# Performance work log

Measured on AMD Instinct MI355X. Metric: run time of the kernel, lower is better.

The kernel has to match this reference:

```python
import jax, jax.numpy as jnp
import numpy as np

B, L, N, H, D, TOPK = 32, 720, 512, 16, 64, 8
TEMP = 1.0


def setup_inputs() -> dict:
    key = jax.random.key(0)
    ks = jax.random.split(key, 18)
    s = lambda k, shp, fan: jax.random.normal(k, shp, jnp.float32) / np.sqrt(fan)
    return {
        'x': jax.random.normal(ks[0], (B, L, N), jnp.float32),
        'var_embed': s(ks[1], (N, H), H),
        'Wq': s(ks[2], (H, H), H), 'bq': jnp.zeros((H,), jnp.float32),
        'Wk': s(ks[3], (H, H), H), 'bk': jnp.zeros((H,), jnp.float32),
        'Wscore': s(ks[4], (N, 1), N), 'bscore': jnp.zeros((1,), jnp.float32),
        'Wc1': s(ks[5], (N, D), N), 'bc1': jnp.zeros((D,), jnp.float32),
        'Wc2': s(ks[6], (D, D), D), 'bc2': jnp.zeros((D,), jnp.float32),
        'Wcn': s(ks[7], (D, N), D), 'bcn': jnp.zeros((N,), jnp.float32),
        'Wg': s(ks[8], (2 * N, N), 2 * N), 'bg': jnp.zeros((N,), jnp.float32),
        'Wf': s(ks[9], (N, N), N), 'bf': jnp.zeros((N,), jnp.float32),
        'gamma': jnp.ones((N,), jnp.float32), 'beta': jnp.zeros((N,), jnp.float32),
    }


def _forward(x, var_embed, Wq, bq, Wk, bk, Wscore, bscore, Wc1, bc1, Wc2, bc2,
             Wcn, bcn, Wg, bg, Wf, bf, gamma, beta):
    # --- SparseVariableRouter (eval mode: no gumbel noise) ---
    Q = var_embed @ Wq + bq          # [N,H]
    K = var_embed @ Wk + bk          # [N,H]
    sim = Q @ K.T                    # [N,N] (identical across batch in torch)
    eye = jnp.eye(N, dtype=bool)
    sim = jnp.where(eye, -1e9, sim)
    topk_vals, topk_idx = jax.lax.top_k(sim, TOPK)      # [N,k]
    w = jax.nn.softmax(topk_vals / TEMP, axis=-1)        # [N,k]
    x_perm = jnp.transpose(x, (0, 2, 1))                 # [B,N,L]
    neighbors = x_perm[:, topk_idx, :]                   # [B,N,k,L] gather
    ring_out = jnp.einsum('bnkl,nk->bln', neighbors, w)  # [B,L,N]
    # --- center path ---
    attn = jax.nn.softmax(x @ Wscore + bscore, axis=1)   # [B,L,1] softmax over L
    center_raw = jnp.sum(x * attn, axis=1)               # [B,N]
    c = jax.nn.gelu(center_raw @ Wc1 + bc1, approximate=False)
    c = jax.nn.gelu(c @ Wc2 + bc2, approximate=False)
    center = c @ Wcn + bcn                               # [B,N]
    center_b = jnp.broadcast_to(center[:, None, :], (x.shape[0], x.shape[1], N))
    # --- gated fusion + residual LN ---
    gate = jax.nn.sigmoid(jnp.concatenate([ring_out, center_b], axis=-1) @ Wg + bg)
    fused = gate * ring_out + (1.0 - gate) * center_b
    fused = fused @ Wf + bf
    h = fused + x
    mu = jnp.mean(h, axis=-1, keepdims=True)
    var = jnp.var(h, axis=-1, keepdims=True)
    return (h - mu) * jax.lax.rsqrt(var + 1e-5) * gamma + beta


def reference(x, var_embed, Wq, bq, Wk, bk, Wscore, bscore, Wc1, bc1, Wc2, bc2,
              Wcn, bcn, Wg, bg, Wf, bf, gamma, beta):
    return _forward(x, var_embed, Wq, bq, Wk, bk, Wscore, bscore, Wc1, bc1,
                    Wc2, bc2, Wcn, bcn, Wg, bg, Wf, bf, gamma, beta)
```

## Files before the change

### kernel.cpp

```cpp
#include <hip/hip_runtime.h>
#include <hip/hip_bf16.h>
#include <math.h>

#define B_ 32
#define L_ 720
#define N_ 512
#define H_ 16
#define D_ 64
#define TOPK_ 8
#define M_ (B_ * L_)
#define RPB 8
#define CRCH 16
#define CRL (L_ / CRCH)
#define OROWS 32

typedef __bf16 bf16x8 __attribute__((ext_vector_type(8)));
typedef float f32x16 __attribute__((ext_vector_type(16)));

__device__ __forceinline__ void async_cp16(const __hip_bfloat16* g, __hip_bfloat16* l) {
    __builtin_amdgcn_global_load_lds(
        (const __attribute__((address_space(1))) void*)g,
        (__attribute__((address_space(3))) void*)l, 16, 0, 0);
}

__device__ __forceinline__ bf16x8 frag_ld(const __hip_bfloat16* base, int row, int j0) {
    return *(const bf16x8*)(base + row * 64 + (((j0) ^ (row & 7)) << 3));
}

__device__ __forceinline__ f32x16 fzero16() {
    f32x16 z;
    #pragma unroll
    for (int e = 0; e < 16; ++e) z[e] = 0.f;
    return z;
}

__global__ __launch_bounds__(512) void prep_kernel(
    const float* __restrict__ Wg, const float* __restrict__ Wf,
    __hip_bfloat16* __restrict__ WgT, __hip_bfloat16* __restrict__ WfPk,
    const float* __restrict__ ve,
    const float* __restrict__ Wq, const float* __restrict__ bq,
    const float* __restrict__ Wk, const float* __restrict__ bk,
    float* __restrict__ Qm, float* __restrict__ Km)
{
    const int bx = blockIdx.x;
    if (bx < 512) {
        const int n = bx;
        const int k = threadIdx.x;
        WgT[n * N_ + k] = __float2bfloat16(Wg[(size_t)k * N_ + n]);
        const int cblk = n >> 5;
        const int ks32 = k >> 4;
        const int l    = (n & 31) + 32 * ((k >> 3) & 1);
        WfPk[(((size_t)cblk * 32 + ks32) * 64 + l) * 8 + (k & 7)] =
            __float2bfloat16(Wf[(size_t)k * N_ + n]);
    } else {
        const int g = (bx - 512) * 512 + threadIdx.x;
        const int j = g >> 4, h = g & 15;
        const float* vr = ve + j * H_;
        float q = bq[h], k = bk[h];
        #pragma unroll
        for (int m = 0; m < H_; ++m) {
            const float v = vr[m];
            q += v * Wq[m * H_ + h];
            k += v * Wk[m * H_ + h];
        }
        Qm[g] = q;
        Km[g] = k;
    }
}

__global__ __launch_bounds__(64) void topk_kernel(
    const float* __restrict__ Qm, const float* __restrict__ Km,
    float* __restrict__ w_out, int* __restrict__ idx_out)
{
    const int n = blockIdx.x;
    const int lane = threadIdx.x;

    float4 q0, q1, q2, q3;
    {
        const float4* qr = (const float4*)(Qm + n * H_);
        q0 = qr[0]; q1 = qr[1]; q2 = qr[2]; q3 = qr[3];
    }

    float sv[8]; int si[8];
    #pragma unroll
    for (int c = 0; c < 8; ++c) {
        const int j = c * 64 + lane;
        const float4* kr = (const float4*)(Km + j * H_);
        float4 k0 = kr[0], k1 = kr[1], k2 = kr[2], k3 = kr[3];
        float s = q0.x * k0.x + q0.y * k0.y + q0.z * k0.z + q0.w * k0.w
                + q1.x * k1.x + q1.y * k1.y + q1.z * k1.z + q1.w * k1.w
                + q2.x * k2.x + q2.y * k2.y + q2.z * k2.z + q2.w * k2.w
                + q3.x * k3.x + q3.y * k3.y + q3.z * k3.z + q3.w * k3.w;
        sv[c] = (j == n) ? -1e9f : s;
        si[c] = j;
    }

    float keepv[TOPK_]; int keepi[TOPK_];
    #pragma unroll
    for (int k = 0; k < TOPK_; ++k) {
        float bv = sv[0]; int bi = si[0]; int bslot = 0;
        #pragma unroll
        for (int c = 1; c < 8; ++c)
            if (sv[c] > bv || (sv[c] == bv && si[c] < bi)) { bv = sv[c]; bi = si[c]; bslot = c; }
        float v = bv; int i = bi;
        #pragma unroll
        for (int off = 32; off > 0; off >>= 1) {
            float v2 = __shfl_xor(v, off);
            int   i2 = __shfl_xor(i, off);
            if (v2 > v || (v2 == v && i2 < i)) { v = v2; i = i2; }
        }
        keepv[k] = v; keepi[k] = i;
        if (i == bi) sv[bslot] = -INFINITY;
    }

    if (lane == 0) {
        float vmax = keepv[0];
        float ev[TOPK_], esum = 0.f;
        #pragma unroll
        for (int k = 0; k < TOPK_; k++) { ev[k] = expf(keepv[k] - vmax); esum += ev[k]; }
        float inv = 1.f / esum;
        #pragma unroll
        for (int k = 0; k < TOPK_; k++) {
            w_out[n * TOPK_ + k] = ev[k] * inv;
            idx_out[n * TOPK_ + k] = keepi[k];
        }
    }
}

__global__ __launch_bounds__(512) void ring_kernel(
    const float* __restrict__ x, const float* __restrict__ w,
    const int* __restrict__ idx,
    const float* __restrict__ Wscore, const float* __restrict__ bscore,
    __hip_bfloat16* __restrict__ ring, float* __restrict__ s)
{
    __shared__ float xs[RPB][N_];
    __shared__ float wsh[N_ * TOPK_];
    __shared__ int   ish[N_ * TOPK_];
    const int t = threadIdx.x;
    const int row0 = blockIdx.x * RPB;

    for (int i = t; i < N_ * TOPK_; i += 512) { wsh[i] = w[i]; ish[i] = idx[i]; }
    {
        const float4* xg = (const float4*)(x + (size_t)row0 * N_);
        float4* xsf = (float4*)&xs[0][0];
        xsf[t] = xg[t];
        xsf[t + 512] = xg[t + 512];
    }
    __syncthreads();

    {
        const int wv = t >> 6, lane = t & 63;
        float sa = 0.f;
        #pragma unroll
        for (int i = 0; i < 8; ++i) sa += xs[wv][lane + i * 64] * Wscore[lane + i * 64];
        for (int off = 32; off > 0; off >>= 1) sa += __shfl_down(sa, off);
        if (lane == 0) s[row0 + wv] = sa + bscore[0];
    }

    float wr[TOPK_]; int ir[TOPK_];
    #pragma unroll
    for (int k = 0; k < TOPK_; ++k) { wr[k] = wsh[t * TOPK_ + k]; ir[k] = ish[t * TOPK_ + k]; }
    #pragma unroll
    for (int r = 0; r < RPB; ++r) {
        float acc = 0.f;
        #pragma unroll
        for (int k = 0; k < TOPK_; ++k) acc += wr[k] * xs[r][ir[k]];
        ring[(size_t)(row0 + r) * N_ + t] = __float2bfloat16(acc);
    }
}

__global__ __launch_bounds__(512) void center_raw_kernel(
    const float* __restrict__ x, const float* __restrict__ s,
    float* __restrict__ craw_p)
{
    const int b = blockIdx.x >> 4;
    const int c = blockIdx.x & 15;
    const int n = threadIdx.x;
    __shared__ float red[8];
    __shared__ float ash[CRL];
    const float* srow = s + (size_t)b * L_;

    float lmax = -1e30f;
    for (int l = n; l < L_; l += 512) lmax = fmaxf(lmax, srow[l]);
    for (int off = 32; off > 0; off >>= 1) lmax = fmaxf(lmax, __shfl_down(lmax, off));
    if ((n & 63) == 0) red[n >> 6] = lmax;
    __syncthreads();
    float gmax = red[0];
    #pragma unroll
    for (int w = 1; w < 8; ++w) gmax = fmaxf(gmax, red[w]);
    __syncthreads();

    float lsum = 0.f;
    for (int l = n; l < L_; l += 512) lsum += expf(srow[l] - gmax);
    for (int off = 32; off > 0; off >>= 1) lsum += __shfl_down(lsum, off);
    if ((n & 63) == 0) red[n >> 6] = lsum;
    __syncthreads();
    float tsum = 0.f;
    #pragma unroll
    for (int w = 0; w < 8; ++w) tsum += red[w];
    const float inv = 1.f / tsum;

    const int l0 = c * CRL;
    if (n < CRL) ash[n] = expf(srow[l0 + n] - gmax) * inv;
    __syncthreads();

    const float* xb = x + ((size_t)b * L_ + l0) * N_;
    float acc = 0.f;
    #pragma unroll 3
    for (int l = 0; l < CRL; l++) acc += ash[l] * xb[(size_t)l * N_ + n];
    craw_p[(size_t)(b * CRCH + c) * N_ + n] = acc;
}

__device__ __forceinline__ float gelu_exact(float v) {
    return 0.5f * v * (1.0f + erff(v * 0.70710678118654752440f));
}

__global__ __launch_bounds__(512) void center_mlp_kernel(
    const float* __restrict__ craw_p,
    const float* __restrict__ Wc1, const float* __restrict__ bc1,
    const float* __restrict__ Wc2, const float* __restrict__ bc2,
    const float* __restrict__ Wcn, const float* __restrict__ bcn,
    float* __restrict__ center)
{
    const int b = blockIdx.x;
    const int t = threadIdx.x;
    const int col = t & 63;
    const int seg = t >> 6;
    __shared__ float cr[N_];
    __shared__ float psum[8][D_];
    __shared__ float h1[D_];
    __shared__ float h2[D_];

    {
        float acc = 0.f;
        #pragma unroll
        for (int c = 0; c < CRCH; ++c) acc += craw_p[(size_t)(b * CRCH + c) * N_ + t];
        cr[t] = acc;
    }
    __syncthreads();
    {
        float p = 0.f;
        #pragma unroll 8
        for (int m = seg * 64; m < seg * 64 + 64; ++m) p += cr[m] * Wc1[m * D_ + col];
        psum[seg][col] = p;
    }
    __syncthreads();
    if (t < D_) {
        float acc = bc1[t];
        #pragma unroll
        for (int s2 = 0; s2 < 8; ++s2) acc += psum[s2][t];
        h1[t] = gelu_exact(acc);
    }
    __syncthreads();
    if (t < D_) {
        float acc = bc2[t];
        #pragma unroll 8
        for (int j = 0; j < D_; j++) acc += h1[j] * Wc2[j * D_ + t];
        h2[t] = gelu_exact(acc);
    }
    __syncthreads();
    {
        float acc = bcn[t];
        #pragma unroll 8
        for (int j = 0; j < D_; j++) acc += h2[j] * Wcn[j * N_ + t];
        center[b * N_ + t] = acc;
    }
}

__global__ __launch_bounds__(512) void cg_kernel(
    const float* __restrict__ center, const float* __restrict__ Wg,
    const float* __restrict__ bg, float* __restrict__ cg)
{
    const int nc = blockIdx.x;
    const int b  = blockIdx.y;
    const int t  = threadIdx.x;
    const int col = nc * 64 + (t & 63);
    const int seg = t >> 6;
    __shared__ float cs[N_];
    __shared__ float psum[8][64];

    cs[t] = center[b * N_ + t];
    __syncthreads();
    {
        float p = 0.f;
        const float* wp = Wg + (size_t)(N_ + seg * 64) * N_ + col;
        #pragma unroll 8
        for (int m = 0; m < 64; ++m) { p += cs[seg * 64 + m] * wp[0]; wp += N_; }
        psum[seg][t & 63] = p;
    }
    __syncthreads();
    if (t < 64) {
        float acc = bg[nc * 64 + t];
        #pragma unroll
        for (int s2 = 0; s2 < 8; ++s2) acc += psum[s2][t];
        cg[b * N_ + nc * 64 + t] = acc;
    }
}

#define GEMM_BODY(EPILOGUE)                                                    \
    __shared__ __hip_bfloat16 Ash[64 * 64];                                    \
    __shared__ __hip_bfloat16 Bsh[64 * 64];                                    \
    const int tid  = threadIdx.x;                                              \
    const int lane = tid & 63;                                                 \
    const int wv   = tid >> 6;                                                 \
    const int m32  = lane & 31;                                                \
    const int half = lane >> 5;                                                \
    const int wr   = wv >> 1;                                                  \
    const int wc   = wv & 1;                                                   \
    const int row0 = blockIdx.x * 64;                                          \
    const int n0   = blockIdx.y * 64;                                          \
    const int swz  = (lane & 7) ^ (lane >> 3);                                 \
    const int rln  = lane >> 3;                                                \
    f32x16 acc;                                                                \
    _Pragma("unroll") for (int e = 0; e < 16; e++) acc[e] = 0.f;               \
    for (int step = 0; step < 8; ++step) {                                     \
        const int k0 = step * 64;                                              \
        const __hip_bfloat16* Ab = A  + (size_t)row0 * N_ + k0 + swz * 8;      \
        const __hip_bfloat16* Bb = BT + (size_t)n0   * N_ + k0 + swz * 8;      \
        __syncthreads();                                                       \
        _Pragma("unroll") for (int j = 0; j < 2; ++j) {                        \
            const int r = j * 32 + wv * 8 + rln;                               \
            const int lb = (j * 256 + wv * 64) * 8;                            \
            async_cp16(Ab + (size_t)r * N_, Ash + lb);                         \
            async_cp16(Bb + (size_t)r * N_, Bsh + lb);                         \
        }                                                                      \
        __syncthreads();                                                       \
        _Pragma("unroll") for (int ks = 0; ks < 4; ++ks) {                     \
            const int j0 = ks * 2 + half;                                      \
            bf16x8 a0 = frag_ld(Ash, wr * 32 + m32, j0);                       \
            bf16x8 b0 = frag_ld(Bsh, wc * 32 + m32, j0);                       \
            acc = __builtin_amdgcn_mfma_f32_32x32x16_bf16(a0, b0, acc, 0, 0, 0); \
        }                                                                      \
    }                                                                          \
    _Pragma("unroll") for (int reg = 0; reg < 16; ++reg) {                     \
        const int rg  = row0 + wr * 32 +                                       \
                        (reg & 3) + 8 * (reg >> 2) + 4 * half;                 \
        const int col = n0 + wc * 32 + m32;                                    \
        const float aval = acc[reg];                                           \
        EPILOGUE                                                               \
    }

__global__ __launch_bounds__(256) void gemm_gate_kernel(
    const __hip_bfloat16* __restrict__ A,
    const __hip_bfloat16* __restrict__ BT,
    const float* __restrict__ cg,
    const float* __restrict__ center,
    __hip_bfloat16* __restrict__ fused)
{
    GEMM_BODY({
        const int bbase = row0 / L_;
        const int b = (rg >= (bbase + 1) * L_) ? bbase + 1 : bbase;
        const float logit = aval + cg[b * N_ + col];
        const float g = 1.f / (1.f + expf(-logit));
        const float rv = __bfloat162float(A[(size_t)rg * N_ + col]);
        const float f = g * rv + (1.f - g) * center[b * N_ + col];
        fused[(size_t)rg * N_ + col] = __float2bfloat16(f);
    })
}

__global__ __launch_bounds__(512) void gemm_out_ln_kernel(
    const __hip_bfloat16* __restrict__ A,
    const __hip_bfloat16* __restrict__ Wpk,
    const float* __restrict__ x,
    const float* __restrict__ bfv,
    const float* __restrict__ gamma,
    const float* __restrict__ beta,
    float* __restrict__ out)
{
    __shared__ __hip_bfloat16 Dsh[2][32 * 64];
    __shared__ float ps[8][32];
    __shared__ float pq[8][32];

    const int tid  = threadIdx.x;
    const int lane = tid & 63;
    const int wv8  = tid >> 6;
    const int m32  = lane & 31;
    const int half = lane >> 5;
    const int row0 = blockIdx.x * OROWS;
    const int swz  = (lane & 7) ^ (lane >> 3);
    const int rln  = lane >> 3;

    f32x16 acc0 = fzero16();
    f32x16 acc1 = fzero16();
    const __hip_bfloat16* wbase = Wpk + ((size_t)(wv8 * 2) * 32 * 64 + lane) * 8;

    if (wv8 < 4) {
        const int r = wv8 * 8 + rln;
        async_cp16(A + (size_t)(row0 + r) * N_ + swz * 8, &Dsh[0][(wv8 * 64) * 8]);
    }
    __syncthreads();
    for (int step = 0; step < 8; ++step) {
        const int cur = step & 1;
        if (step < 7 && wv8 < 4) {
            const int r = wv8 * 8 + rln;
            async_cp16(A + (size_t)(row0 + r) * N_ + (step + 1) * 64 + swz * 8,
                       &Dsh[cur ^ 1][(wv8 * 64) * 8]);
        }
        #pragma unroll
        for (int ks = 0; ks < 4; ++ks) {
            const int j0   = ks * 2 + half;
            const int ks32 = step * 4 + ks;
            bf16x8 d0 = frag_ld(Dsh[cur], m32, j0);
            bf16x8 wa = *(const bf16x8*)(wbase + (size_t)ks32 * 64 * 8);
            bf16x8 wb = *(const bf16x8*)(wbase + (size_t)(32 * 64 + ks32 * 64) * 8);
            acc0 = __builtin_amdgcn_mfma_f32_32x32x16_bf16(wa, d0, acc0, 0, 0, 0);
            acc1 = __builtin_amdgcn_mfma_f32_32x32x16_bf16(wb, d0, acc1, 0, 0, 0);
        }
        __syncthreads();
    }

    const int rowg = row0 + m32;
    float ls = 0.f, lq = 0.f;
#define OEPI2(AC, I)                                                           \
    {                                                                          \
        const int ntb = (wv8 * 2 + (I)) * 32;                                  \
        _Pragma("unroll") for (int q = 0; q < 4; ++q) {                        \
            const int nb = ntb + 8 * q + 4 * half;                             \
            const float4 bq = *(const float4*)(bfv + nb);                      \
            const float4 xq = *(const float4*)(x + (size_t)rowg * N_ + nb);    \
            AC[4 * q + 0] += bq.x + xq.x;                                      \
            AC[4 * q + 1] += bq.y + xq.y;                                      \
            AC[4 * q + 2] += bq.z + xq.z;                                      \
            AC[4 * q + 3] += bq.w + xq.w;                                      \
            ls += AC[4 * q + 0] + AC[4 * q + 1] + AC[4 * q + 2] + AC[4 * q + 3]; \
            lq += AC[4 * q + 0] * AC[4 * q + 0] + AC[4 * q + 1] * AC[4 * q + 1]  \
                + AC[4 * q + 2] * AC[4 * q + 2] + AC[4 * q + 3] * AC[4 * q + 3]; \
        }                                                                      \
    }
    OEPI2(acc0, 0) OEPI2(acc1, 1)

    ls += __shfl_xor(ls, 32);
    lq += __shfl_xor(lq, 32);
    if (half == 0) { ps[wv8][m32] = ls; pq[wv8][m32] = lq; }
    __syncthreads();

    float S = 0.f, Q2 = 0.f;
    #pragma unroll
    for (int w = 0; w < 8; ++w) { S += ps[w][m32]; Q2 += pq[w][m32]; }
    const float mu  = S * (1.0f / N_);
    const float var = Q2 * (1.0f / N_) - mu * mu;
    const float inv = rsqrtf(var + 1e-5f);

#define LSTORE2(AC, I)                                                         \
    {                                                                          \
        const int ntb = (wv8 * 2 + (I)) * 32;                                  \
        _Pragma("unroll") for (int q = 0; q < 4; ++q) {                        \
            const int nb = ntb + 8 * q + 4 * half;                             \
            const float4 g4 = *(const float4*)(gamma + nb);                    \
            const float4 b4 = *(const float4*)(beta + nb);                     \
            float4 o;                                                          \
            o.x = (AC[4 * q + 0] - mu) * inv * g4.x + b4.x;                    \
            o.y = (AC[4 * q + 1] - mu) * inv * g4.y + b4.y;                    \
            o.z = (AC[4 * q + 2] - mu) * inv * g4.z + b4.z;                    \
            o.w = (AC[4 * q + 3] - mu) * inv * g4.w + b4.w;                    \
            *(float4*)(out + (size_t)rowg * N_ + nb) = o;                      \
        }                                                                      \
    }
    LSTORE2(acc0, 0) LSTORE2(acc1, 1)
}

extern "C" void kernel_launch(void* const* d_in, const int* in_sizes, int n_in,
                              void* d_out, int out_size, void* d_ws, size_t ws_size,
                              hipStream_t stream) {
    const float* x       = (const float*)d_in[0];
    const float* ve      = (const float*)d_in[1];
    const float* Wq      = (const float*)d_in[2];
    const float* bq      = (const float*)d_in[3];
    const float* Wk      = (const float*)d_in[4];
    const float* bk      = (const float*)d_in[5];
    const float* Wscore  = (const float*)d_in[6];
    const float* bscore  = (const float*)d_in[7];
    const float* Wc1     = (const float*)d_in[8];
    const float* bc1     = (const float*)d_in[9];
    const float* Wc2     = (const float*)d_in[10];
    const float* bc2     = (const float*)d_in[11];
    const float* Wcn     = (const float*)d_in[12];
    const float* bcn     = (const float*)d_in[13];
    const float* Wg      = (const float*)d_in[14];
    const float* bg      = (const float*)d_in[15];
    const float* Wf      = (const float*)d_in[16];
    const float* bf      = (const float*)d_in[17];
    const float* gamma   = (const float*)d_in[18];
    const float* beta    = (const float*)d_in[19];
    float* out = (float*)d_out;

    char* p = (char*)d_ws;
    float* ws_w    = (float*)p; p += N_ * TOPK_ * sizeof(float);
    int*   ws_idx  = (int*)p;   p += N_ * TOPK_ * sizeof(int);
    float* ws_s    = (float*)p; p += B_ * L_ * sizeof(float);
    float* ws_crp  = (float*)p; p += B_ * CRCH * N_ * sizeof(float);
    float* ws_cent = (float*)p; p += B_ * N_ * sizeof(float);
    float* ws_cg   = (float*)p; p += B_ * N_ * sizeof(float);
    float* ws_Q    = (float*)p; p += N_ * H_ * sizeof(float);
    float* ws_K    = (float*)p; p += N_ * H_ * sizeof(float);
    __hip_bfloat16* ws_ring  = (__hip_bfloat16*)p; p += (size_t)M_ * N_ * sizeof(__hip_bfloat16);
    __hip_bfloat16* ws_fused = (__hip_bfloat16*)p; p += (size_t)M_ * N_ * sizeof(__hip_bfloat16);
    __hip_bfloat16* ws_WgT   = (__hip_bfloat16*)p; p += (size_t)N_ * N_ * sizeof(__hip_bfloat16);
    __hip_bfloat16* ws_WfPk  = (__hip_bfloat16*)p; p += (size_t)N_ * N_ * sizeof(__hip_bfloat16);

    prep_kernel<<<528, 512, 0, stream>>>(Wg, Wf, ws_WgT, ws_WfPk,
                                         ve, Wq, bq, Wk, bk, ws_Q, ws_K);
    topk_kernel<<<N_, 64, 0, stream>>>(ws_Q, ws_K, ws_w, ws_idx);
    ring_kernel<<<M_ / RPB, 512, 0, stream>>>(x, ws_w, ws_idx, Wscore, bscore,
                                              ws_ring, ws_s);
    center_raw_kernel<<<B_ * CRCH, 512, 0, stream>>>(x, ws_s, ws_crp);
    center_mlp_kernel<<<B_, 512, 0, stream>>>(ws_crp, Wc1, bc1, Wc2, bc2,
                                              Wcn, bcn, ws_cent);
    cg_kernel<<<dim3(8, B_), 512, 0, stream>>>(ws_cent, Wg, bg, ws_cg);
    dim3 ggrid(M_ / 64, N_ / 64);
    gemm_gate_kernel<<<ggrid, 256, 0, stream>>>(ws_ring, ws_WgT, ws_cg,
                                                ws_cent, ws_fused);
    gemm_out_ln_kernel<<<M_ / OROWS, 512, 0, stream>>>(ws_fused, ws_WfPk, x, bf,
                                                       gamma, beta, out);
}
```

Measured before the change: 252.9 us.

## Fuse gate GEMM and output GEMM+LayerNorm into one tail kernel

Merges the gate GEMM (with sigmoid blend) and the output GEMM with LayerNorm into a single kernel that handles 32 full rows per block. The ring rows are loaded once into a 32KB swizzled LDS tile, the fused result overwrites that tile in place, and the second GEMM reads it from LDS. This removes the global write and read of the bf16 fused intermediate and one launch. Wg is now stored in the same packed layout as Wf. The cost is more LDS per block, which may reduce occupancy, and the full 512-column weights are streamed from global/L2 by every block.

```diff
diff --git a/kernel.cpp b/kernel.cpp
--- a/kernel.cpp
+++ b/kernel.cpp
@@ -12,7 +12,7 @@
 #define RPB 8
 #define CRCH 16
 #define CRL (L_ / CRCH)
-#define OROWS 32
+#define PROWS 32
 
 typedef __bf16 bf16x8 __attribute__((ext_vector_type(8)));
 typedef float f32x16 __attribute__((ext_vector_type(16)));
@@ -23,10 +23,6 @@
         (__attribute__((address_space(3))) void*)l, 16, 0, 0);
 }
 
-__device__ __forceinline__ bf16x8 frag_ld(const __hip_bfloat16* base, int row, int j0) {
-    return *(const bf16x8*)(base + row * 64 + (((j0) ^ (row & 7)) << 3));
-}
-
 __device__ __forceinline__ f32x16 fzero16() {
     f32x16 z;
     #pragma unroll
@@ -34,9 +30,15 @@
     return z;
 }
 
+__device__ __forceinline__ bf16x8 rsh_ld(const __hip_bfloat16* base, int row, int c8) {
+    return *(const bf16x8*)(base + row * 512 + ((c8 ^ (row & 31)) << 3));
+}
+
+__device__ __forceinline__ float sigm(float v) { return 1.f / (1.f + expf(-v)); }
+
 __global__ __launch_bounds__(512) void prep_kernel(
     const float* __restrict__ Wg, const float* __restrict__ Wf,
-    __hip_bfloat16* __restrict__ WgT, __hip_bfloat16* __restrict__ WfPk,
+    __hip_bfloat16* __restrict__ WgPk, __hip_bfloat16* __restrict__ WfPk,
     const float* __restrict__ ve,
     const float* __restrict__ Wq, const float* __restrict__ bq,
     const float* __restrict__ Wk, const float* __restrict__ bk,
@@ -46,12 +48,12 @@
     if (bx < 512) {
         const int n = bx;
         const int k = threadIdx.x;
-        WgT[n * N_ + k] = __float2bfloat16(Wg[(size_t)k * N_ + n]);
         const int cblk = n >> 5;
         const int ks32 = k >> 4;
         const int l    = (n & 31) + 32 * ((k >> 3) & 1);
-        WfPk[(((size_t)cblk * 32 + ks32) * 64 + l) * 8 + (k & 7)] =
-            __float2bfloat16(Wf[(size_t)k * N_ + n]);
+        const size_t pkidx = (((size_t)cblk * 32 + ks32) * 64 + l) * 8 + (k & 7);
+        WgPk[pkidx] = __float2bfloat16(Wg[(size_t)k * N_ + n]);
+        WfPk[pkidx] = __float2bfloat16(Wf[(size_t)k * N_ + n]);
     } else {
         const int g = (bx - 512) * 512 + threadIdx.x;
         const int j = g >> 4, h = g & 15;
@@ -297,77 +299,21 @@
     }
 }
 
-#define GEMM_BODY(EPILOGUE)                                                    \
-    __shared__ __hip_bfloat16 Ash[64 * 64];                                    \
-    __shared__ __hip_bfloat16 Bsh[64 * 64];                                    \
-    const int tid  = threadIdx.x;                                              \
-    const int lane = tid & 63;                                                 \
-    const int wv   = tid >> 6;                                                 \
-    const int m32  = lane & 31;                                                \
-    const int half = lane >> 5;                                                \
-    const int wr   = wv >> 1;                                                  \
-    const int wc   = wv & 1;                                                   \
-    const int row0 = blockIdx.x * 64;                                          \
-    const int n0   = blockIdx.y * 64;                                          \
-    const int swz  = (lane & 7) ^ (lane >> 3);                                 \
-    const int rln  = lane >> 3;                                                \
-    f32x16 acc;                                                                \
-    _Pragma("unroll") for (int e = 0; e < 16; e++) acc[e] = 0.f;               \
-    for (int step = 0; step < 8; ++step) {                                     \
-        const int k0 = step * 64;                                              \
-        const __hip_bfloat16* Ab = A  + (size_t)row0 * N_ + k0 + swz * 8;      \
-        const __hip_bfloat16* Bb = BT + (size_t)n0   * N_ + k0 + swz * 8;      \
-        __syncthreads();                                                       \
-        _Pragma("unroll") for (int j = 0; j < 2; ++j) {                        \
-            const int r = j * 32 + wv * 8 + rln;                               \
-            const int lb = (j * 256 + wv * 64) * 8;                            \
-            async_cp16(Ab + (size_t)r * N_, Ash + lb);                         \
-            async_cp16(Bb + (size_t)r * N_, Bsh + lb);                         \
-        }                                                                      \
-        __syncthreads();                                                       \
-        _Pragma("unroll") for (int ks = 0; ks < 4; ++ks) {                     \
-            const int j0 = ks * 2 + half;                                      \
-            bf16x8 a0 = frag_ld(Ash, wr * 32 + m32, j0);                       \
-            bf16x8 b0 = frag_ld(Bsh, wc * 32 + m32, j0);                       \
-            acc = __builtin_amdgcn_mfma_f32_32x32x16_bf16(a0, b0, acc, 0, 0, 0); \
-        }                                                                      \
-    }                                                                          \
-    _Pragma("unroll") for (int reg = 0; reg < 16; ++reg) {                     \
-        const int rg  = row0 + wr * 32 +                                       \
-                        (reg & 3) + 8 * (reg >> 2) + 4 * half;                 \
-        const int col = n0 + wc * 32 + m32;                                    \
-        const float aval = acc[reg];                                           \
-        EPILOGUE                                                               \
-    }
-
-__global__ __launch_bounds__(256) void gemm_gate_kernel(
-    const __hip_bfloat16* __restrict__ A,
-    const __hip_bfloat16* __restrict__ BT,
+__global__ __launch_bounds__(512) void tail_kernel(
+    const __hip_bfloat16* __restrict__ ring,
+    const __hip_bfloat16* __restrict__ WgPk,
+    const __hip_bfloat16* __restrict__ WfPk,
     const float* __restrict__ cg,
     const float* __restrict__ center,
-    __hip_bfloat16* __restrict__ fused)
-{
-    GEMM_BODY({
-        const int bbase = row0 / L_;
-        const int b = (rg >= (bbase + 1) * L_) ? bbase + 1 : bbase;
-        const float logit = aval + cg[b * N_ + col];
-        const float g = 1.f / (1.f + expf(-logit));
-        const float rv = __bfloat162float(A[(size_t)rg * N_ + col]);
-        const float f = g * rv + (1.f - g) * center[b * N_ + col];
-        fused[(size_t)rg * N_ + col] = __float2bfloat16(f);
-    })
-}
-
-__global__ __launch_bounds__(512) void gemm_out_ln_kernel(
-    const __hip_bfloat16* __restrict__ A,
-    const __hip_bfloat16* __restrict__ Wpk,
     const float* __restrict__ x,
     const float* __restrict__ bfv,
     const float* __restrict__ gamma,
     const float* __restrict__ beta,
     float* __restrict__ out)
 {
-    __shared__ __hip_bfloat16 Dsh[2][32 * 64];
+    __shared__ __attribute__((aligned(16))) __hip_bfloat16 Rsh[PROWS * N_];
+    __shared__ float cgs[2][N_];
+    __shared__ float cents[2][N_];
     __shared__ float ps[8][32];
     __shared__ float pq[8][32];
 
@@ -376,40 +322,89 @@
     const int wv8  = tid >> 6;
     const int m32  = lane & 31;
     const int half = lane >> 5;
-    const int row0 = blockIdx.x * OROWS;
-    const int swz  = (lane & 7) ^ (lane >> 3);
-    const int rln  = lane >> 3;
-
-    f32x16 acc0 = fzero16();
-    f32x16 acc1 = fzero16();
-    const __hip_bfloat16* wbase = Wpk + ((size_t)(wv8 * 2) * 32 * 64 + lane) * 8;
-
-    if (wv8 < 4) {
-        const int r = wv8 * 8 + rln;
-        async_cp16(A + (size_t)(row0 + r) * N_ + swz * 8, &Dsh[0][(wv8 * 64) * 8]);
-    }
-    __syncthreads();
-    for (int step = 0; step < 8; ++step) {
-        const int cur = step & 1;
-        if (step < 7 && wv8 < 4) {
-            const int r = wv8 * 8 + rln;
-            async_cp16(A + (size_t)(row0 + r) * N_ + (step + 1) * 64 + swz * 8,
-                       &Dsh[cur ^ 1][(wv8 * 64) * 8]);
-        }
-        #pragma unroll
-        for (int ks = 0; ks < 4; ++ks) {
-            const int j0   = ks * 2 + half;
-            const int ks32 = step * 4 + ks;
-            bf16x8 d0 = frag_ld(Dsh[cur], m32, j0);
+    const int row0 = blockIdx.x * PROWS;
+    const int b0   = row0 / L_;
+    const int b1   = (row0 + PROWS - 1) / L_;
+    const int rowg = row0 + m32;
+    const int bsel = (rowg / L_ != b0) ? 1 : 0;
+
+    for (int i = tid; i < N_; i += 512) {
+        cgs[0][i]   = cg[b0 * N_ + i];
+        cgs[1][i]   = cg[b1 * N_ + i];
+        cents[0][i] = center[b0 * N_ + i];
+        cents[1][i] = center[b1 * N_ + i];
+    }
+    #pragma unroll
+    for (int r = 0; r < 4; ++r) {
+        const int row = r * 8 + wv8;
+        const int c8s = lane ^ (row & 31);
+        async_cp16(ring + (size_t)(row0 + row) * N_ + c8s * 8,
+                   Rsh + row * 512);
+    }
+    __syncthreads();
+
+    f32x16 ga0 = fzero16(), ga1 = fzero16();
+    {
+        const __hip_bfloat16* wbase = WgPk + ((size_t)(wv8 * 2) * 32 * 64 + lane) * 8;
+        #pragma unroll 8
+        for (int ks32 = 0; ks32 < 32; ++ks32) {
+            const int c8 = ks32 * 2 + half;
+            bf16x8 d0 = rsh_ld(Rsh, m32, c8);
             bf16x8 wa = *(const bf16x8*)(wbase + (size_t)ks32 * 64 * 8);
             bf16x8 wb = *(const bf16x8*)(wbase + (size_t)(32 * 64 + ks32 * 64) * 8);
-            acc0 = __builtin_amdgcn_mfma_f32_32x32x16_bf16(wa, d0, acc0, 0, 0, 0);
-            acc1 = __builtin_amdgcn_mfma_f32_32x32x16_bf16(wb, d0, acc1, 0, 0, 0);
+            ga0 = __builtin_amdgcn_mfma_f32_32x32x16_bf16(wa, d0, ga0, 0, 0, 0);
+            ga1 = __builtin_amdgcn_mfma_f32_32x32x16_bf16(wb, d0, ga1, 0, 0, 0);
         }
-        __syncthreads();
-    }
-
-    const int rowg = row0 + m32;
+    }
+    __syncthreads();
+
+#define GEPI(AC, I)                                                            \
+    {                                                                          \
+        const int ntb = (wv8 * 2 + (I)) * 32;                                  \
+        _Pragma("unroll") for (int q = 0; q < 4; ++q) {                        \
+            const int nb = ntb + 8 * q + 4 * half;                             \
+            const float4 cgq = *(const float4*)&cgs[bsel][nb];                 \
+            const float4 ctq = *(const float4*)&cents[bsel][nb];               \
+            __hip_bfloat16* slot = Rsh + m32 * 512 +                           \
+                                   (((nb >> 3) ^ m32) << 3) + (nb & 7);        \
+            const uint2 rvp = *(const uint2*)slot;                             \
+            const float rv0 = __uint_as_float((rvp.x & 0xffffu) << 16);        \
+            const float rv1 = __uint_as_float((rvp.x >> 16) << 16);            \
+            const float rv2 = __uint_as_float((rvp.y & 0xffffu) << 16);        \
+            const float rv3 = __uint_as_float((rvp.y >> 16) << 16);            \
+            const float g0 = sigm(AC[4 * q + 0] + cgq.x);                      \
+            const float g1 = sigm(AC[4 * q + 1] + cgq.y);                      \
+            const float g2 = sigm(AC[4 * q + 2] + cgq.z);                      \
+            const float g3 = sigm(AC[4 * q + 3] + cgq.w);                      \
+            const float f0 = g0 * rv0 + (1.f - g0) * ctq.x;                    \
+            const float f1 = g1 * rv1 + (1.f - g1) * ctq.y;                    \
+            const float f2 = g2 * rv2 + (1.f - g2) * ctq.z;                    \
+            const float f3 = g3 * rv3 + (1.f - g3) * ctq.w;                    \
+            uint2 wpk;                                                         \
+            wpk.x = (unsigned)__builtin_bit_cast(unsigned short, __float2bfloat16(f0)) |        \
+                    ((unsigned)__builtin_bit_cast(unsigned short, __float2bfloat16(f1)) << 16); \
+            wpk.y = (unsigned)__builtin_bit_cast(unsigned short, __float2bfloat16(f2)) |        \
+                    ((unsigned)__builtin_bit_cast(unsigned short, __float2bfloat16(f3)) << 16); \
+            *(uint2*)slot = wpk;                                               \
+        }                                                                      \
+    }
+    GEPI(ga0, 0) GEPI(ga1, 1)
+    __syncthreads();
+
+    f32x16 oc0 = fzero16(), oc1 = fzero16();
+    {
+        const __hip_bfloat16* wbase = WfPk + ((size_t)(wv8 * 2) * 32 * 64 + lane) * 8;
+        #pragma unroll 8
+        for (int ks32 = 0; ks32 < 32; ++ks32) {
+            const int c8 = ks32 * 2 + half;
+            bf16x8 d0 = rsh_ld(Rsh, m32, c8);
+            bf16x8 wa = *(const bf16x8*)(wbase + (size_t)ks32 * 64 * 8);
+            bf16x8 wb = *(const bf16x8*)(wbase + (size_t)(32 * 64 + ks32 * 64) * 8);
+            oc0 = __builtin_amdgcn_mfma_f32_32x32x16_bf16(wa, d0, oc0, 0, 0, 0);
+            oc1 = __builtin_amdgcn_mfma_f32_32x32x16_bf16(wb, d0, oc1, 0, 0, 0);
+        }
+    }
+
     float ls = 0.f, lq = 0.f;
 #define OEPI2(AC, I)                                                           \
     {                                                                          \
@@ -427,7 +422,7 @@
                 + AC[4 * q + 2] * AC[4 * q + 2] + AC[4 * q + 3] * AC[4 * q + 3]; \
         }                                                                      \
     }
-    OEPI2(acc0, 0) OEPI2(acc1, 1)
+    OEPI2(oc0, 0) OEPI2(oc1, 1)
 
     ls += __shfl_xor(ls, 32);
     lq += __shfl_xor(lq, 32);
@@ -456,7 +451,7 @@
             *(float4*)(out + (size_t)rowg * N_ + nb) = o;                      \
         }                                                                      \
     }
-    LSTORE2(acc0, 0) LSTORE2(acc1, 1)
+    LSTORE2(oc0, 0) LSTORE2(oc1, 1)
 }
 
 extern "C" void kernel_launch(void* const* d_in, const int* in_sizes, int n_in,
@@ -494,11 +489,10 @@
     float* ws_Q    = (float*)p; p += N_ * H_ * sizeof(float);
     float* ws_K    = (float*)p; p += N_ * H_ * sizeof(float);
     __hip_bfloat16* ws_ring  = (__hip_bfloat16*)p; p += (size_t)M_ * N_ * sizeof(__hip_bfloat16);
-    __hip_bfloat16* ws_fused = (__hip_bfloat16*)p; p += (size_t)M_ * N_ * sizeof(__hip_bfloat16);
-    __hip_bfloat16* ws_WgT   = (__hip_bfloat16*)p; p += (size_t)N_ * N_ * sizeof(__hip_bfloat16);
+    __hip_bfloat16* ws_WgPk  = (__hip_bfloat16*)p; p += (size_t)N_ * N_ * sizeof(__hip_bfloat16);
     __hip_bfloat16* ws_WfPk  = (__hip_bfloat16*)p; p += (size_t)N_ * N_ * sizeof(__hip_bfloat16);
 
-    prep_kernel<<<528, 512, 0, stream>>>(Wg, Wf, ws_WgT, ws_WfPk,
+    prep_kernel<<<528, 512, 0, stream>>>(Wg, Wf, ws_WgPk, ws_WfPk,
                                          ve, Wq, bq, Wk, bk, ws_Q, ws_K);
     topk_kernel<<<N_, 64, 0, stream>>>(ws_Q, ws_K, ws_w, ws_idx);
     ring_kernel<<<M_ / RPB, 512, 0, stream>>>(x, ws_w, ws_idx, Wscore, bscore,
@@ -507,9 +501,7 @@
     center_mlp_kernel<<<B_, 512, 0, stream>>>(ws_crp, Wc1, bc1, Wc2, bc2,
                                               Wcn, bcn, ws_cent);
     cg_kernel<<<dim3(8, B_), 512, 0, stream>>>(ws_cent, Wg, bg, ws_cg);
-    dim3 ggrid(M_ / 64, N_ / 64);
-    gemm_gate_kernel<<<ggrid, 256, 0, stream>>>(ws_ring, ws_WgT, ws_cg,
-                                                ws_cent, ws_fused);
-    gemm_out_ln_kernel<<<M_ / OROWS, 512, 0, stream>>>(ws_fused, ws_WfPk, x, bf,
-                                                       gamma, beta, out);
-}
+    tail_kernel<<<M_ / PROWS, 512, 0, stream>>>(ws_ring, ws_WgPk, ws_WfPk,
+                                                ws_cg, ws_cent, x, bf,
+                                                gamma, beta, out);
+}
```

Result: faster. 247.5 us (-2.2%).
